# Kernel tuning notes

Hardware: AMD Instinct MI355X
Metric: run time of the kernel (lower is better)

## Reference

```python
import jax, jax.numpy as jnp
import numpy as np

INPUT_DIM = 512
N_TREES = 64
TREE_DEPTH = 3
N_LEAVES = 2 ** TREE_DEPTH      # 8
N_INTERNAL = 2 ** TREE_DEPTH - 1  # 7
PPT = N_INTERNAL * (INPUT_DIM + 1) + N_LEAVES * 2  # params per tree = 3607
BATCH = 65536


def setup_inputs() -> dict:
    key = jax.random.key(0)
    k1, k2, k3 = jax.random.split(key, 3)
    x = jax.random.normal(k1, (BATCH, INPUT_DIM), dtype=jnp.float32)
    tree_params = jax.random.normal(k2, (1, N_TREES * PPT), dtype=jnp.float32)
    tree_weights = jax.random.normal(k3, (1, N_TREES), dtype=jnp.float32)
    return {"x": x, "tree_params": tree_params, "tree_weights": tree_weights}


def reference(x, tree_params, tree_weights):
    # Unpack all trees at once: [T, ppt]
    p = tree_params[0].reshape(N_TREES, PPT)
    split_w = p[:, : N_INTERNAL * INPUT_DIM].reshape(N_TREES, N_INTERNAL, INPUT_DIM)
    split_b = p[:, N_INTERNAL * INPUT_DIM : N_INTERNAL * (INPUT_DIM + 1)]  # [T, I]
    leaf_logits = p[:, N_INTERNAL * (INPUT_DIM + 1) :].reshape(N_TREES, N_LEAVES, 2)

    # decisions: [B, T, I]
    decisions = jax.nn.sigmoid(jnp.einsum('bd,tid->bti', x, split_w) + split_b[None])

    # Replicate the original indexing quirk: leaf_probs column j (a tree NODE index)
    # gets factor d_i if j == 2i+1 (and j < n_leaves), (1-d_i) if j == 2i+2.
    # Column 0 remains 1.0; each other column gets exactly one factor.
    cols = []
    for j in range(N_LEAVES):
        if j == 0:
            cols.append(jnp.ones_like(decisions[:, :, 0]))
        elif j % 2 == 1:
            i = (j - 1) // 2
            cols.append(decisions[:, :, i] if i < N_INTERNAL else jnp.ones_like(decisions[:, :, 0]))
        else:
            i = (j - 2) // 2
            cols.append(1.0 - decisions[:, :, i] if i < N_INTERNAL else jnp.ones_like(decisions[:, :, 0]))
    leaf_probs = jnp.stack(cols, axis=-1)  # [B, T, L]
    leaf_probs = leaf_probs / (leaf_probs.sum(axis=-1, keepdims=True) + 1e-8)

    leaf_dist = jax.nn.softmax(leaf_logits, axis=-1)  # [T, L, 2]
    tree_out = jnp.einsum('btl,tlc->btc', leaf_probs, leaf_dist)  # [B, T, 2]
    return jnp.einsum('btc,t->bc', tree_out, tree_weights[0])  # [B, 2]
```

## Files before the change

### kernel.cpp

```cpp
#include <hip/hip_runtime.h>
#include <stdint.h>


#define BATCH 65536
#define KDIM 512
#define NCOL 256
#define PPT 3607

typedef _Float16 f16x8 __attribute__((ext_vector_type(8)));
typedef float f32x4 __attribute__((ext_vector_type(4)));


__global__ __launch_bounds__(128) void prep_kernel(const float* __restrict__ p,
                                                   const float* __restrict__ tw,
                                                   _Float16* __restrict__ Wh,
                                                   float* __restrict__ biasN,
                                                   float* __restrict__ AB) {
    const int c = blockIdx.x;
    const int t = c >> 2, i = c & 3;
    const float* wsrc = p + t * PPT + i * KDIM;
    for (int k = threadIdx.x; k < KDIM; k += 128)
        Wh[c * KDIM + k] = (_Float16)wsrc[k];
    if (threadIdx.x == 0)
        biasN[c] = p[t * PPT + 7 * KDIM + i];
    if (threadIdx.x == 64 && c < 64) {
        const int tt = c;
        const float* lg = p + tt * PPT + 7 * 513;
        const float w = tw[tt];
        float ld[8][2];
#pragma unroll
        for (int j = 0; j < 8; ++j) {
            float a = lg[2 * j], b = lg[2 * j + 1];
            float m = fmaxf(a, b);
            float e0 = expf(a - m), e1 = expf(b - m);
            float s = e0 + e1;
            ld[j][0] = e0 / s; ld[j][1] = e1 / s;
        }
        float* o = AB + tt * 10;
#pragma unroll
        for (int cc = 0; cc < 2; ++cc) {
            o[0 + cc] = w * (ld[0][cc] + ld[2][cc] + ld[4][cc] + ld[6][cc]);
            o[2 + cc] = w * (ld[1][cc] - ld[2][cc]);
            o[4 + cc] = w * (ld[3][cc] - ld[4][cc]);
            o[6 + cc] = w * (ld[5][cc] - ld[6][cc]);
            o[8 + cc] = w * (ld[7][cc]);
        }
    }
}

#define AB_LDS 33920
#define PART_LDS 32896

__global__ __launch_bounds__(512, 2) void main_kernel(const float* __restrict__ X,
                                                      const _Float16* __restrict__ Wh,
                                                      const float* __restrict__ biasN,
                                                      const float* __restrict__ ABg,
                                                      float* __restrict__ out) {
    extern __shared__ char smem[];
    _Float16* lds_h = (_Float16*)smem;
    float* lds_f = (float*)smem;

    const int tid = threadIdx.x;
    const int lane = tid & 63;
    const int wid = tid >> 6;
    const int wm = wid >> 2;
    const int wn = wid & 3;
    const int gr0 = blockIdx.x * 256;

#pragma unroll
    for (int i = 0; i < 2; ++i) {
        int idx = tid + i * 512;
        if (idx < 640) lds_f[AB_LDS + idx] = ABg[idx];
    }

    f32x4 acc[8][4];
#pragma unroll
    for (int rt = 0; rt < 8; ++rt)
#pragma unroll
        for (int nt = 0; nt < 4; ++nt)
            acc[rt][nt] = (f32x4){0.f, 0.f, 0.f, 0.f};

    const int arow = tid >> 1;
    const int akq = (tid & 1) * 32;
    const int sw = (arow & 7) << 3;
    const float* Xrow = X + (size_t)(gr0 + arow) * KDIM + akq;
    const _Float16* Wrow = Wh + (size_t)arow * KDIM + akq;

    float4 ar[8];
    uint4 br[4];

#pragma unroll
    for (int j = 0; j < 8; ++j) ar[j] = *(const float4*)(Xrow + j * 4);
#pragma unroll
    for (int j = 0; j < 4; ++j) br[j] = *(const uint4*)(Wrow + j * 8);
#pragma unroll
    for (int j2 = 0; j2 < 4; ++j2) {
        const float4 u = ar[j2 * 2], v = ar[j2 * 2 + 1];
        f16x8 h;
        h[0] = (_Float16)u.x; h[1] = (_Float16)u.y; h[2] = (_Float16)u.z; h[3] = (_Float16)u.w;
        h[4] = (_Float16)v.x; h[5] = (_Float16)v.y; h[6] = (_Float16)v.z; h[7] = (_Float16)v.w;
        int k0 = akq + j2 * 8;
        *(f16x8*)&lds_h[arow * 64 + (k0 ^ sw)] = h;
        *(uint4*)&lds_h[16384 + arow * 64 + (k0 ^ sw)] = br[j2];
    }
    __syncthreads();

    int cur = 0;
    for (int kt = 0; kt < 8; ++kt) {
        if (kt < 7) {
#pragma unroll
            for (int j = 0; j < 8; ++j) ar[j] = *(const float4*)(Xrow + (kt + 1) * 64 + j * 4);
#pragma unroll
            for (int j = 0; j < 4; ++j) br[j] = *(const uint4*)(Wrow + (kt + 1) * 64 + j * 8);
        }
        const int bb = cur * 32768;
#pragma unroll
        for (int k32 = 0; k32 < 2; ++k32) {
            const int kb = k32 * 32 + ((lane >> 4) << 3);
            f16x8 bfr[4];
#pragma unroll
            for (int nt = 0; nt < 4; ++nt) {
                int col = wn * 64 + nt * 16 + (lane & 15);
                bfr[nt] = *(const f16x8*)&lds_h[bb + 16384 + col * 64 + (kb ^ ((col & 7) << 3))];
            }
#pragma unroll
            for (int rt = 0; rt < 8; ++rt) {
                int row = wm * 128 + rt * 16 + (lane & 15);
                f16x8 afr = *(const f16x8*)&lds_h[bb + row * 64 + (kb ^ ((row & 7) << 3))];
#pragma unroll
                for (int nt = 0; nt < 4; ++nt)
                    acc[rt][nt] = __builtin_amdgcn_mfma_f32_16x16x32_f16(afr, bfr[nt], acc[rt][nt], 0, 0, 0);
            }
        }
        if (kt < 7) {
            const int nb = (cur ^ 1) * 32768;
#pragma unroll
            for (int j2 = 0; j2 < 4; ++j2) {
                const float4 u = ar[j2 * 2], v = ar[j2 * 2 + 1];
                f16x8 h;
                h[0] = (_Float16)u.x; h[1] = (_Float16)u.y; h[2] = (_Float16)u.z; h[3] = (_Float16)u.w;
                h[4] = (_Float16)v.x; h[5] = (_Float16)v.y; h[6] = (_Float16)v.z; h[7] = (_Float16)v.w;
                int k0 = akq + j2 * 8;
                *(f16x8*)&lds_h[nb + arow * 64 + (k0 ^ sw)] = h;
                *(uint4*)&lds_h[nb + 16384 + arow * 64 + (k0 ^ sw)] = br[j2];
            }
        }
        __syncthreads();
        cur ^= 1;
    }

    float bias_l[4];
#pragma unroll
    for (int nt = 0; nt < 4; ++nt) bias_l[nt] = biasN[wn * 64 + nt * 16 + (lane & 15)];

    for (int pp = 0; pp < 2; ++pp) {
        if (wm == pp) {
#pragma unroll
            for (int rt = 0; rt < 8; ++rt)
#pragma unroll
                for (int nt = 0; nt < 4; ++nt) {
                    int col = wn * 64 + nt * 16 + (lane & 15);
#pragma unroll
                    for (int reg = 0; reg < 4; ++reg) {
                        int row = rt * 16 + ((lane >> 4) << 2) + reg;
                        float z = acc[rt][nt][reg] + bias_l[nt];
                        float d = __builtin_amdgcn_rcpf(1.f + __expf(-z));
                        lds_f[row * 257 + col] = d;
                    }
                }
        }
        __syncthreads();
        {
            const int g = tid >> 7, row = tid & 127;
            float o0 = 0.f, o1 = 0.f;
#pragma unroll
            for (int ttl = 0; ttl < 16; ++ttl) {
                int t = g * 16 + ttl;
                const float* dp = lds_f + row * 257 + t * 4;
                float d0 = dp[0], d1 = dp[1], d2 = dp[2], d3 = dp[3];
                const float* abt = lds_f + AB_LDS + t * 10;
                float inv = __builtin_amdgcn_rcpf(4.f + d3 + 1e-8f);
                o0 += (abt[0] + d0 * abt[2] + d1 * abt[4] + d2 * abt[6] + d3 * abt[8]) * inv;
                o1 += (abt[1] + d0 * abt[3] + d1 * abt[5] + d2 * abt[7] + d3 * abt[9]) * inv;
            }
            lds_f[PART_LDS + (g * 128 + row) * 2 + 0] = o0;
            lds_f[PART_LDS + (g * 128 + row) * 2 + 1] = o1;
        }
        __syncthreads();
        if (tid < 256) {
            int r = tid >> 1, c = tid & 1;
            float s = 0.f;
#pragma unroll
            for (int g2 = 0; g2 < 4; ++g2) s += lds_f[PART_LDS + (g2 * 128 + r) * 2 + c];
            out[(size_t)(gr0 + pp * 128 + r) * 2 + c] = s;
        }
        if (pp == 0) __syncthreads();
    }
}

extern "C" void kernel_launch(void* const* d_in, const int* in_sizes, int n_in,
                              void* d_out, int out_size, void* d_ws, size_t ws_size,
                              hipStream_t stream) {
    const float* x  = (const float*)d_in[0];
    const float* tp = (const float*)d_in[1];
    const float* tw = (const float*)d_in[2];
    float* out = (float*)d_out;

    _Float16* Wh = (_Float16*)d_ws;
    float* biasN = (float*)((char*)d_ws + 262144);
    float* AB    = (float*)((char*)d_ws + 263168);

    (void)hipFuncSetAttribute((const void*)reinterpret_cast<const void*>(&main_kernel),
                              hipFuncAttributeMaxDynamicSharedMemorySize, 138240);

    prep_kernel<<<256, 128, 0, stream>>>(tp, tw, Wh, biasN, AB);
    main_kernel<<<256, 512, 138240, stream>>>(x, Wh, biasN, AB, out);
}
```

Before: 48.33 us.

## Stream X and W into LDS via direct global_load_lds with smaller tiles

```diff
diff --git a/kernel.cpp b/kernel.cpp
--- a/kernel.cpp
+++ b/kernel.cpp
@@ -2,9 +2,7 @@
 #include <stdint.h>
 
 
-#define BATCH 65536
 #define KDIM 512
-#define NCOL 256
 #define PPT 3607
 
 typedef _Float16 f16x8 __attribute__((ext_vector_type(8)));
@@ -48,154 +46,161 @@
     }
 }
 
-#define AB_LDS 33920
-#define PART_LDS 32896
-
-__global__ __launch_bounds__(512, 2) void main_kernel(const float* __restrict__ X,
+#define BUF_STRIDE 32768
+#define W_OFF 16384
+#define EPI_STRIDE 260
+#define AB_OFF 66560
+#define PART_OFF 69120
+#define LDS_BYTES 73216
+
+__device__ __forceinline__ void gll16(const void* g, void* l) {
+    __builtin_amdgcn_global_load_lds((const __attribute__((address_space(1))) uint32_t*)g,
+                                     (__attribute__((address_space(3))) uint32_t*)l, 16, 0, 0);
+}
+
+__global__ __launch_bounds__(512, 4) void main_kernel(const float* __restrict__ X,
                                                       const _Float16* __restrict__ Wh,
                                                       const float* __restrict__ biasN,
                                                       const float* __restrict__ ABg,
                                                       float* __restrict__ out) {
     extern __shared__ char smem[];
-    _Float16* lds_h = (_Float16*)smem;
-    float* lds_f = (float*)smem;
-
     const int tid = threadIdx.x;
     const int lane = tid & 63;
-    const int wid = tid >> 6;
-    const int wm = wid >> 2;
-    const int wn = wid & 3;
-    const int gr0 = blockIdx.x * 256;
-
+    const int w = tid >> 6;
+    const int wm = w >> 2;
+    const int wn = w & 3;
+    const int gr0 = blockIdx.x * 128;
+
+    {
+        float* abl = (float*)(smem + AB_OFF);
+        for (int i = tid; i < 640; i += 512) abl[i] = ABg[i];
+    }
+    asm volatile("s_waitcnt vmcnt(0)" ::: "memory");
+
+    const float* srcX[2];
+    const _Float16* srcW[2];
+    int ldoX[2], ldoW[2];
 #pragma unroll
     for (int i = 0; i < 2; ++i) {
-        int idx = tid + i * 512;
-        if (idx < 640) lds_f[AB_LDS + idx] = ABg[idx];
-    }
-
-    f32x4 acc[8][4];
-#pragma unroll
-    for (int rt = 0; rt < 8; ++rt)
+        int rowX = i * 64 + w * 8 + (lane >> 3);
+        int cX = ((lane & 7) << 2) ^ ((rowX & 7) << 2);
+        srcX[i] = X + (size_t)(gr0 + rowX) * KDIM + cX;
+        ldoX[i] = (i * 512 + w * 64 + lane) * 16;
+        int colW = i * 128 + w * 16 + (lane >> 2);
+        int kW = ((lane & 3) << 3) ^ (((colW >> 1) & 3) << 3);
+        srcW[i] = Wh + (size_t)colW * KDIM + kW;
+        ldoW[i] = W_OFF + (i * 512 + w * 64 + lane) * 16;
+    }
+
+#define STAGE(kt, b) do {                                   \
+        char* _bb = smem + (b) * BUF_STRIDE;                \
+        gll16(srcX[0] + (kt) * 32, _bb + ldoX[0]);          \
+        gll16(srcX[1] + (kt) * 32, _bb + ldoX[1]);          \
+        gll16(srcW[0] + (kt) * 32, _bb + ldoW[0]);          \
+        gll16(srcW[1] + (kt) * 32, _bb + ldoW[1]);          \
+    } while (0)
+
+    f32x4 acc[4][4];
+#pragma unroll
+    for (int rt = 0; rt < 4; ++rt)
 #pragma unroll
         for (int nt = 0; nt < 4; ++nt)
             acc[rt][nt] = (f32x4){0.f, 0.f, 0.f, 0.f};
 
-    const int arow = tid >> 1;
-    const int akq = (tid & 1) * 32;
-    const int sw = (arow & 7) << 3;
-    const float* Xrow = X + (size_t)(gr0 + arow) * KDIM + akq;
-    const _Float16* Wrow = Wh + (size_t)arow * KDIM + akq;
-
-    float4 ar[8];
-    uint4 br[4];
-
-#pragma unroll
-    for (int j = 0; j < 8; ++j) ar[j] = *(const float4*)(Xrow + j * 4);
-#pragma unroll
-    for (int j = 0; j < 4; ++j) br[j] = *(const uint4*)(Wrow + j * 8);
-#pragma unroll
-    for (int j2 = 0; j2 < 4; ++j2) {
-        const float4 u = ar[j2 * 2], v = ar[j2 * 2 + 1];
-        f16x8 h;
-        h[0] = (_Float16)u.x; h[1] = (_Float16)u.y; h[2] = (_Float16)u.z; h[3] = (_Float16)u.w;
-        h[4] = (_Float16)v.x; h[5] = (_Float16)v.y; h[6] = (_Float16)v.z; h[7] = (_Float16)v.w;
-        int k0 = akq + j2 * 8;
-        *(f16x8*)&lds_h[arow * 64 + (k0 ^ sw)] = h;
-        *(uint4*)&lds_h[16384 + arow * 64 + (k0 ^ sw)] = br[j2];
-    }
+    const int kb = (lane >> 4) << 3;
+    const int swA = (lane & 7) << 2;
+    const int swB = ((lane >> 1) & 3) << 3;
+    const int aRowBase = (wm * 64 + (lane & 15)) * 32;
+    const int bColBase = (wn * 64 + (lane & 15)) * 32;
+
+    STAGE(0, 0);
+
+    for (int kt = 0; kt < 16; ++kt) {
+        const int b = kt & 1;
+        __builtin_amdgcn_s_barrier();
+        if (kt < 15) {
+            STAGE(kt + 1, b ^ 1);
+            asm volatile("s_waitcnt vmcnt(4)" ::: "memory");
+        } else {
+            asm volatile("s_waitcnt vmcnt(0)" ::: "memory");
+        }
+        __builtin_amdgcn_s_barrier();
+        asm volatile("" ::: "memory");
+
+        const float* Xl = (const float*)(smem + b * BUF_STRIDE);
+        const _Float16* Wl = (const _Float16*)(smem + b * BUF_STRIDE + W_OFF);
+
+        f16x8 bfr[4];
+#pragma unroll
+        for (int nt = 0; nt < 4; ++nt)
+            bfr[nt] = *(const f16x8*)&Wl[bColBase + nt * 512 + (kb ^ swB)];
+#pragma unroll
+        for (int rt = 0; rt < 4; ++rt) {
+            float4 a0 = *(const float4*)&Xl[aRowBase + rt * 512 + (kb ^ swA)];
+            float4 a1 = *(const float4*)&Xl[aRowBase + rt * 512 + ((kb + 4) ^ swA)];
+            f16x8 af;
+            af[0] = (_Float16)a0.x; af[1] = (_Float16)a0.y;
+            af[2] = (_Float16)a0.z; af[3] = (_Float16)a0.w;
+            af[4] = (_Float16)a1.x; af[5] = (_Float16)a1.y;
+            af[6] = (_Float16)a1.z; af[7] = (_Float16)a1.w;
+#pragma unroll
+            for (int nt = 0; nt < 4; ++nt)
+                acc[rt][nt] = __builtin_amdgcn_mfma_f32_16x16x32_f16(af, bfr[nt], acc[rt][nt], 0, 0, 0);
+        }
+    }
+
     __syncthreads();
 
-    int cur = 0;
-    for (int kt = 0; kt < 8; ++kt) {
-        if (kt < 7) {
-#pragma unroll
-            for (int j = 0; j < 8; ++j) ar[j] = *(const float4*)(Xrow + (kt + 1) * 64 + j * 4);
-#pragma unroll
-            for (int j = 0; j < 4; ++j) br[j] = *(const uint4*)(Wrow + (kt + 1) * 64 + j * 8);
-        }
-        const int bb = cur * 32768;
-#pragma unroll
-        for (int k32 = 0; k32 < 2; ++k32) {
-            const int kb = k32 * 32 + ((lane >> 4) << 3);
-            f16x8 bfr[4];
-#pragma unroll
-            for (int nt = 0; nt < 4; ++nt) {
-                int col = wn * 64 + nt * 16 + (lane & 15);
-                bfr[nt] = *(const f16x8*)&lds_h[bb + 16384 + col * 64 + (kb ^ ((col & 7) << 3))];
-            }
-#pragma unroll
-            for (int rt = 0; rt < 8; ++rt) {
-                int row = wm * 128 + rt * 16 + (lane & 15);
-                f16x8 afr = *(const f16x8*)&lds_h[bb + row * 64 + (kb ^ ((row & 7) << 3))];
-#pragma unroll
-                for (int nt = 0; nt < 4; ++nt)
-                    acc[rt][nt] = __builtin_amdgcn_mfma_f32_16x16x32_f16(afr, bfr[nt], acc[rt][nt], 0, 0, 0);
-            }
-        }
-        if (kt < 7) {
-            const int nb = (cur ^ 1) * 32768;
-#pragma unroll
-            for (int j2 = 0; j2 < 4; ++j2) {
-                const float4 u = ar[j2 * 2], v = ar[j2 * 2 + 1];
-                f16x8 h;
-                h[0] = (_Float16)u.x; h[1] = (_Float16)u.y; h[2] = (_Float16)u.z; h[3] = (_Float16)u.w;
-                h[4] = (_Float16)v.x; h[5] = (_Float16)v.y; h[6] = (_Float16)v.z; h[7] = (_Float16)v.w;
-                int k0 = akq + j2 * 8;
-                *(f16x8*)&lds_h[nb + arow * 64 + (k0 ^ sw)] = h;
-                *(uint4*)&lds_h[nb + 16384 + arow * 64 + (k0 ^ sw)] = br[j2];
-            }
-        }
-        __syncthreads();
-        cur ^= 1;
-    }
-
-    float bias_l[4];
-#pragma unroll
-    for (int nt = 0; nt < 4; ++nt) bias_l[nt] = biasN[wn * 64 + nt * 16 + (lane & 15)];
-
-    for (int pp = 0; pp < 2; ++pp) {
-        if (wm == pp) {
-#pragma unroll
-            for (int rt = 0; rt < 8; ++rt)
+    for (int p = 0; p < 2; ++p) {
+        if (wm == p) {
+            float bl[4];
+#pragma unroll
+            for (int nt = 0; nt < 4; ++nt) bl[nt] = biasN[wn * 64 + nt * 16 + (lane & 15)];
+            float* ep = (float*)smem;
+#pragma unroll
+            for (int rt = 0; rt < 4; ++rt)
 #pragma unroll
                 for (int nt = 0; nt < 4; ++nt) {
-                    int col = wn * 64 + nt * 16 + (lane & 15);
+                    const int col = wn * 64 + nt * 16 + (lane & 15);
 #pragma unroll
                     for (int reg = 0; reg < 4; ++reg) {
-                        int row = rt * 16 + ((lane >> 4) << 2) + reg;
-                        float z = acc[rt][nt][reg] + bias_l[nt];
-                        float d = __builtin_amdgcn_rcpf(1.f + __expf(-z));
-                        lds_f[row * 257 + col] = d;
+                        const int rowl = rt * 16 + ((lane >> 4) << 2) + reg;
+                        float z = acc[rt][nt][reg] + bl[nt];
+                        ep[rowl * EPI_STRIDE + col] = __builtin_amdgcn_rcpf(1.f + __expf(-z));
                     }
                 }
         }
         __syncthreads();
         {
-            const int g = tid >> 7, row = tid & 127;
-            float o0 = 0.f, o1 = 0.f;
-#pragma unroll
-            for (int ttl = 0; ttl < 16; ++ttl) {
-                int t = g * 16 + ttl;
-                const float* dp = lds_f + row * 257 + t * 4;
-                float d0 = dp[0], d1 = dp[1], d2 = dp[2], d3 = dp[3];
-                const float* abt = lds_f + AB_LDS + t * 10;
-                float inv = __builtin_amdgcn_rcpf(4.f + d3 + 1e-8f);
-                o0 += (abt[0] + d0 * abt[2] + d1 * abt[4] + d2 * abt[6] + d3 * abt[8]) * inv;
-                o1 += (abt[1] + d0 * abt[3] + d1 * abt[5] + d2 * abt[7] + d3 * abt[9]) * inv;
+            const float* ep = (const float*)smem;
+            const float* abl = (const float*)(smem + AB_OFF);
+            float* pb = (float*)(smem + PART_OFF);
+            const int r = lane;
+            float s0 = 0.f, s1 = 0.f;
+#pragma unroll
+            for (int j = 0; j < 8; ++j) {
+                const int t = w * 8 + j;
+                float4 dv = *(const float4*)&ep[r * EPI_STRIDE + t * 4];
+                const float* abt = &abl[t * 10];
+                float inv = __builtin_amdgcn_rcpf(4.f + dv.w + 1e-8f);
+                s0 += (abt[0] + dv.x * abt[2] + dv.y * abt[4] + dv.z * abt[6] + dv.w * abt[8]) * inv;
+                s1 += (abt[1] + dv.x * abt[3] + dv.y * abt[5] + dv.z * abt[7] + dv.w * abt[9]) * inv;
             }
-            lds_f[PART_LDS + (g * 128 + row) * 2 + 0] = o0;
-            lds_f[PART_LDS + (g * 128 + row) * 2 + 1] = o1;
+            pb[(w * 64 + r) * 2 + 0] = s0;
+            pb[(w * 64 + r) * 2 + 1] = s1;
         }
         __syncthreads();
-        if (tid < 256) {
-            int r = tid >> 1, c = tid & 1;
+        if (tid < 128) {
+            const float* pb = (const float*)(smem + PART_OFF);
+            const int r = tid >> 1, c = tid & 1;
             float s = 0.f;
 #pragma unroll
-            for (int g2 = 0; g2 < 4; ++g2) s += lds_f[PART_LDS + (g2 * 128 + r) * 2 + c];
-            out[(size_t)(gr0 + pp * 128 + r) * 2 + c] = s;
-        }
-        if (pp == 0) __syncthreads();
-    }
+            for (int g = 0; g < 8; ++g) s += pb[(g * 64 + r) * 2 + c];
+            out[(size_t)(gr0 + p * 64 + r) * 2 + c] = s;
+        }
+        if (p == 0) __syncthreads();
+    }
+#undef STAGE
 }
 
 extern "C" void kernel_launch(void* const* d_in, const int* in_sizes, int n_in,
@@ -211,8 +216,8 @@
     float* AB    = (float*)((char*)d_ws + 263168);
 
     (void)hipFuncSetAttribute((const void*)reinterpret_cast<const void*>(&main_kernel),
-                              hipFuncAttributeMaxDynamicSharedMemorySize, 138240);
+                              hipFuncAttributeMaxDynamicSharedMemorySize, LDS_BYTES);
 
     prep_kernel<<<256, 128, 0, stream>>>(tp, tw, Wh, biasN, AB);
-    main_kernel<<<256, 512, 138240, stream>>>(x, Wh, biasN, AB, out);
-}
+    main_kernel<<<512, 512, LDS_BYTES, stream>>>(x, Wh, biasN, AB, out);
+}
```

Result: faster. 41.93 us (-13.2%).
